# Optimization experiments

Hardware: AMD Instinct MI355X
Metric: run time of the kernel (lower is better)

The kernel has to match this reference:

```python
import jax, jax.numpy as jnp
import numpy as np

TOP_K = 2


def setup_inputs() -> dict:
    key = jax.random.key(0)
    ks = jax.random.split(key, 8)
    B, S, D, E = 4, 2048, 768, 8
    F = 4 * D
    scale = 0.02
    x = jax.random.normal(ks[0], (B, S, D), dtype=jnp.float32)
    router_w = jax.random.normal(ks[1], (D, E), dtype=jnp.float32) * scale
    router_b = jnp.zeros((E,), dtype=jnp.float32)
    w1 = jax.random.normal(ks[2], (E, D, F), dtype=jnp.float32) * scale
    b1 = jnp.zeros((E, F), dtype=jnp.float32)
    w2 = jax.random.normal(ks[3], (E, F, D), dtype=jnp.float32) * scale
    b2 = jnp.zeros((E, D), dtype=jnp.float32)
    return {"x": x, "router_w": router_w, "router_b": router_b,
            "w1": w1, "b1": b1, "w2": w2, "b2": b2}


def reference(x, router_w, router_b, w1, b1, w2, b2):
    E = w1.shape[0]
    # router: [B,S,E]
    logits = jnp.einsum('bsd,de->bse', x, router_w) + router_b
    probs = jax.nn.softmax(logits, axis=-1)
    top_p, top_i = jax.lax.top_k(probs, TOP_K)          # [B,S,K]
    top_p = top_p / jnp.sum(top_p, axis=-1, keepdims=True)
    # dense combine weights [B,S,E]: renormalized top-k prob if selected else 0
    combine = jnp.sum(jax.nn.one_hot(top_i, E, dtype=x.dtype) * top_p[..., None], axis=-2)
    # loop over small fixed expert count (structurally distinct weight slices)
    out = jnp.zeros_like(x)
    for e in range(E):
        h = jax.nn.gelu(jnp.einsum('bsd,df->bsf', x, w1[e]) + b1[e], approximate=False)
        y = jnp.einsum('bsf,fd->bsd', h, w2[e]) + b2[e]
        out = out + combine[..., e:e + 1] * y
    return out
```

## Files before the change

### kernel.cpp

```cpp
#include <hip/hip_runtime.h>
#include <hip/hip_bf16.h>
#include <math.h>

#define TOKENS 8192
#define Dm 768
#define Fm 3072
#define Em 8
#define BK 64
#define MT_MAX 71

typedef __attribute__((ext_vector_type(8))) short short8v;
typedef __attribute__((ext_vector_type(4))) short short4v;
typedef __attribute__((ext_vector_type(4))) float f32x4;

__device__ inline short f2b(float f) {
  __hip_bfloat16 h = __float2bfloat16(f);
  return *reinterpret_cast<short*>(&h);
}

__device__ inline void async16(short* lds, const short* g) {
  __builtin_amdgcn_global_load_lds((const __attribute__((address_space(1))) void*)g,
                                   (__attribute__((address_space(3))) void*)lds, 16, 0, 0);
}

__global__ __launch_bounds__(256) void cvt_tr_kernel(const float* __restrict__ in,
                                                     short* __restrict__ out, int R, int C) {
  __shared__ short tile[64][68];
  size_t eoff = (size_t)blockIdx.z * R * C;
  const float* inp = in + eoff;
  short* outp = out + eoff;
  int tc = blockIdx.x * 64, tr = blockIdx.y * 64;
  {
    int row = threadIdx.x >> 2;
    int cch = (threadIdx.x & 3) * 16;
    const float* src = inp + (size_t)(tr + row) * C + tc + cch;
    #pragma unroll
    for (int q = 0; q < 4; q++) {
      float4 v = *(const float4*)(src + q * 4);
      tile[row][cch + q * 4 + 0] = f2b(v.x);
      tile[row][cch + q * 4 + 1] = f2b(v.y);
      tile[row][cch + q * 4 + 2] = f2b(v.z);
      tile[row][cch + q * 4 + 3] = f2b(v.w);
    }
  }
  __syncthreads();
  {
    int c = threadIdx.x >> 2;
    int rch = (threadIdx.x & 3) * 16;
    short tmp[16];
    #pragma unroll
    for (int i = 0; i < 16; i++) tmp[i] = tile[rch + i][c];
    short* dst = outp + (size_t)(tc + c) * R + tr + rch;
    *(short8v*)(dst) = *(short8v*)(tmp);
    *(short8v*)(dst + 8) = *(short8v*)(tmp + 8);
  }
}

__global__ __launch_bounds__(256) void router_kernel(
    const float* __restrict__ x, const float* __restrict__ rw,
    const float* __restrict__ rb, const float* __restrict__ b2,
    short* __restrict__ xb, float* __restrict__ out,
    int2* __restrict__ meta_e, float2* __restrict__ meta_p) {
  int wave = threadIdx.x >> 6;
  int lane = threadIdx.x & 63;
  int t = blockIdx.x * 4 + wave;
  if (t >= TOKENS) return;
  const float* xr = x + (size_t)t * Dm;
  short* xbr = xb + (size_t)t * Dm;
  float acc[Em];
  #pragma unroll
  for (int e = 0; e < Em; e++) acc[e] = 0.f;
  #pragma unroll
  for (int i = 0; i < 3; i++) {
    int d = i * 256 + lane * 4;
    float4 v = *(const float4*)(xr + d);
    short4v s;
    s[0] = f2b(v.x); s[1] = f2b(v.y); s[2] = f2b(v.z); s[3] = f2b(v.w);
    *(short4v*)(xbr + d) = s;
    #pragma unroll
    for (int j = 0; j < 4; j++) {
      float xv = (j == 0) ? v.x : (j == 1) ? v.y : (j == 2) ? v.z : v.w;
      const float4* rwp = (const float4*)(rw + (size_t)(d + j) * Em);
      float4 a = rwp[0], b = rwp[1];
      acc[0] += xv * a.x; acc[1] += xv * a.y; acc[2] += xv * a.z; acc[3] += xv * a.w;
      acc[4] += xv * b.x; acc[5] += xv * b.y; acc[6] += xv * b.z; acc[7] += xv * b.w;
    }
  }
  #pragma unroll
  for (int e = 0; e < Em; e++) {
    float v = acc[e];
    #pragma unroll
    for (int s = 32; s > 0; s >>= 1) v += __shfl_xor(v, s);
    acc[e] = v + rb[e];
  }
  int i1 = 0; float m1 = acc[0];
  #pragma unroll
  for (int e = 1; e < Em; e++) if (acc[e] > m1) { m1 = acc[e]; i1 = e; }
  int i2 = -1; float m2 = -1e30f;
  #pragma unroll
  for (int e = 0; e < Em; e++) if (e != i1 && acc[e] > m2) { m2 = acc[e]; i2 = e; }
  float tt = expf(m2 - m1);
  float p0 = 1.f / (1.f + tt);
  float p1 = tt / (1.f + tt);
  const float4* ba = (const float4*)(b2 + (size_t)i1 * Dm);
  const float4* bb = (const float4*)(b2 + (size_t)i2 * Dm);
  float4* orow = (float4*)(out + (size_t)t * Dm);
  #pragma unroll
  for (int i = 0; i < 3; i++) {
    int idx = lane + 64 * i;
    float4 a = ba[idx], b = bb[idx];
    float4 o;
    o.x = p0 * a.x + p1 * b.x; o.y = p0 * a.y + p1 * b.y;
    o.z = p0 * a.z + p1 * b.z; o.w = p0 * a.w + p1 * b.w;
    orow[idx] = o;
  }
  if (lane == 0) {
    meta_e[t] = make_int2(i1, i2);
    meta_p[t] = make_float2(p0, p1);
  }
}

__global__ __launch_bounds__(256) void scatter_kernel(
    const int2* __restrict__ meta_e, const float2* __restrict__ meta_p,
    int* __restrict__ cnt, int* __restrict__ list, float* __restrict__ wlist) {
  __shared__ int lcnt[Em];
  __shared__ int gbase[Em];
  int t = blockIdx.x * 256 + threadIdx.x;
  if (threadIdx.x < Em) lcnt[threadIdx.x] = 0;
  __syncthreads();
  int2 e = meta_e[t];
  float2 p = meta_p[t];
  int r0 = atomicAdd(&lcnt[e.x], 1);
  int r1 = atomicAdd(&lcnt[e.y], 1);
  __syncthreads();
  if (threadIdx.x < Em) gbase[threadIdx.x] = atomicAdd(&cnt[threadIdx.x], lcnt[threadIdx.x]);
  __syncthreads();
  int s0 = gbase[e.x] + r0;
  int s1 = gbase[e.y] + r1;
  list[e.x * TOKENS + s0] = t;  wlist[e.x * TOKENS + s0] = p.x;
  list[e.y * TOKENS + s1] = t;  wlist[e.y * TOKENS + s1] = p.y;
}

__global__ void prefix_kernel(const int* __restrict__ cnt, int* __restrict__ hoffs,
                              int2* __restrict__ table, int* __restrict__ ntab) {
  if (threadIdx.x == 0) {
    int s = 0, k = 0;
    for (int e = 0; e < Em; e++) {
      hoffs[e] = s;
      int c = cnt[e];
      for (int mb = 0; mb < c; mb += 256) table[k++] = make_int2(e, mb);
      s += c;
    }
    ntab[0] = k;
  }
}

template <int MODE, int NB>
__global__ __launch_bounds__(512, 2) void moe_gemm_kernel(
    const short* __restrict__ Abase, const short* __restrict__ Wt,
    const float* __restrict__ bias, short* __restrict__ Hout,
    float* __restrict__ Out, const int* __restrict__ cnt,
    const int* __restrict__ hoffs, const int* __restrict__ list,
    const float* __restrict__ wlist, const int2* __restrict__ table,
    const int* __restrict__ ntab, int Ndim, int Kdim) {
  int nwg = gridDim.x;
  int orig = blockIdx.x;
  int q8 = nwg >> 3, r8 = nwg & 7, xcd = orig & 7;
  int wg = (xcd < r8 ? xcd * (q8 + 1) : r8 * (q8 + 1) + (xcd - r8) * q8) + (orig >> 3);
  int ti = wg / NB, nt = wg % NB;
  if (ti >= ntab[0]) return;
  int2 te = table[ti];
  int e = te.x, mbase = te.y;
  int count = cnt[e], ho = hoffs[e];
  int n0 = nt * 256;

  __shared__ short As[2][256 * 64];
  __shared__ short Bs[2][256 * 64];
  __shared__ int rid_s[256];
  __shared__ float pw_s[256];

  int tid = threadIdx.x;
  if (tid < 256) {
    int rc = mbase + tid; if (rc > count - 1) rc = count - 1;
    rid_s[tid] = list[e * TOKENS + rc];
    pw_s[tid] = wlist[e * TOKENS + rc];
  }
  __syncthreads();

  const short* We = Wt + (size_t)e * Ndim * Kdim;
  const short* aptr[4];
  const short* bptr[4];
  #pragma unroll
  for (int q = 0; q < 4; q++) {
    int r = q * 64 + (tid >> 3);
    int g = (tid & 7) ^ (r & 7);
    size_t grow;
    if (MODE == 0) {
      grow = (size_t)rid_s[r] * Kdim;
    } else {
      int rr = mbase + r; if (rr > count - 1) rr = count - 1;
      grow = (size_t)(ho + rr) * Kdim;
    }
    aptr[q] = Abase + grow + g * 8;
    bptr[q] = We + (size_t)(n0 + r) * Kdim + g * 8;
  }
  int w = tid >> 6;

  #define STAGE(s)                                             \
    {                                                          \
      _Pragma("unroll")                                        \
      for (int q = 0; q < 4; q++) {                            \
        async16(&As[s][q * 4096 + w * 512], aptr[q]); aptr[q] += BK; \
        async16(&Bs[s][q * 4096 + w * 512], bptr[q]); bptr[q] += BK; \
      }                                                        \
      __builtin_amdgcn_sched_barrier(0);                       \
    }

  int NT = Kdim / BK;
  f32x4 acc[8][4] = {};
  int lane = tid & 63;
  int wm = (tid >> 6) >> 2, wn = (tid >> 6) & 3;
  int lr = lane & 15, lh = lane >> 4;
  int rsw = lr & 7;

  STAGE(0);
  __syncthreads();
  for (int t = 0; t < NT; t++) {
    int cur = t & 1;
    if (t + 1 < NT) STAGE(cur ^ 1);
    const short* Ab = As[cur];
    const short* Bb = Bs[cur];
    #pragma unroll
    for (int kk = 0; kk < 2; kk++) {
      short8v a[8], b[4];
      #pragma unroll
      for (int m = 0; m < 8; m++)
        a[m] = *(const short8v*)&Ab[(wm * 128 + m * 16 + lr) * 64 + ((kk * 4 + lh) ^ rsw) * 8];
      #pragma unroll
      for (int n = 0; n < 4; n++)
        b[n] = *(const short8v*)&Bb[(wn * 64 + n * 16 + lr) * 64 + ((kk * 4 + lh) ^ rsw) * 8];
      #pragma unroll
      for (int m = 0; m < 8; m++)
        #pragma unroll
        for (int n = 0; n < 4; n++)
          acc[m][n] = __builtin_amdgcn_mfma_f32_16x16x32_bf16(a[m], b[n], acc[m][n], 0, 0, 0);
    }
    __syncthreads();
  }
  #undef STAGE

  if (MODE == 0) {
    const float* be = bias + (size_t)e * Ndim;
    #pragma unroll
    for (int m = 0; m < 8; m++) {
      #pragma unroll
      for (int j = 0; j < 4; j++) {
        int r = wm * 128 + m * 16 + lh * 4 + j;
        if (mbase + r < count) {
          size_t rowoff = (size_t)(ho + mbase + r) * Ndim;
          #pragma unroll
          for (int n = 0; n < 4; n++) {
            int colg = n0 + wn * 64 + n * 16 + lr;
            float val = acc[m][n][j] + be[colg];
            float z = val * 0.70710678118654752f;
            float az = fabsf(z);
            float tt = __fdividef(1.f, fmaf(0.3275911f, az, 1.f));
            float poly = fmaf(fmaf(fmaf(fmaf(1.061405429f, tt, -1.453152027f), tt,
                              1.421413741f), tt, -0.284496736f), tt, 0.254829592f) * tt;
            float er = 1.f - poly * __expf(-az * az);
            er = z < 0.f ? -er : er;
            val = 0.5f * val * (1.f + er);
            Hout[rowoff + colg] = f2b(val);
          }
        }
      }
    }
  } else {
    #pragma unroll
    for (int m = 0; m < 8; m++) {
      #pragma unroll
      for (int j = 0; j < 4; j++) {
        int r = wm * 128 + m * 16 + lh * 4 + j;
        if (mbase + r < count) {
          float* orow = Out + (size_t)rid_s[r] * Dm;
          float p = pw_s[r];
          #pragma unroll
          for (int n = 0; n < 4; n++) {
            int colg = n0 + wn * 64 + n * 16 + lr;
            atomicAdd(&orow[colg], p * acc[m][n][j]);
          }
        }
      }
    }
  }
}

extern "C" void kernel_launch(void* const* d_in, const int* in_sizes, int n_in,
                              void* d_out, int out_size, void* d_ws, size_t ws_size,
                              hipStream_t stream) {
  const float* x  = (const float*)d_in[0];
  const float* rw = (const float*)d_in[1];
  const float* rb = (const float*)d_in[2];
  const float* w1 = (const float*)d_in[3];
  const float* b1 = (const float*)d_in[4];
  const float* w2 = (const float*)d_in[5];
  const float* b2 = (const float*)d_in[6];
  float* out = (float*)d_out;
  char* ws = (char*)d_ws;

  const size_t off_cnt    = 0;
  const size_t off_hoffs  = 64;
  const size_t off_ntab   = 128;
  const size_t off_table  = 192;
  const size_t off_list   = 2048;
  const size_t off_wlist  = off_list + (size_t)Em * TOKENS * 4;
  const size_t off_meta_e = off_wlist + (size_t)Em * TOKENS * 4;
  const size_t off_meta_p = off_meta_e + (size_t)TOKENS * 8;
  const size_t off_xbf    = off_meta_p + (size_t)TOKENS * 8;
  const size_t off_w1t    = off_xbf + (size_t)TOKENS * Dm * 2;
  const size_t off_w2t    = off_w1t + (size_t)Em * Dm * Fm * 2;
  const size_t off_h      = off_w2t + (size_t)Em * Fm * Dm * 2;
  const size_t needed     = off_h + (size_t)2 * TOKENS * Fm * 2;
  if (ws_size < needed) return;

  int*    cnt    = (int*)(ws + off_cnt);
  int*    hoffs  = (int*)(ws + off_hoffs);
  int*    ntab   = (int*)(ws + off_ntab);
  int2*   table  = (int2*)(ws + off_table);
  int*    list   = (int*)(ws + off_list);
  float*  wlist  = (float*)(ws + off_wlist);
  int2*   meta_e = (int2*)(ws + off_meta_e);
  float2* meta_p = (float2*)(ws + off_meta_p);
  short*  xbf    = (short*)(ws + off_xbf);
  short*  w1t    = (short*)(ws + off_w1t);
  short*  w2t    = (short*)(ws + off_w2t);
  short*  h      = (short*)(ws + off_h);

  hipMemsetAsync(cnt, 0, 32, stream);
  cvt_tr_kernel<<<dim3(Fm / 64, Dm / 64, Em), 256, 0, stream>>>(w1, w1t, Dm, Fm);
  cvt_tr_kernel<<<dim3(Dm / 64, Fm / 64, Em), 256, 0, stream>>>(w2, w2t, Fm, Dm);
  router_kernel<<<TOKENS / 4, 256, 0, stream>>>(x, rw, rb, b2, xbf, out, meta_e, meta_p);
  scatter_kernel<<<TOKENS / 256, 256, 0, stream>>>(meta_e, meta_p, cnt, list, wlist);
  prefix_kernel<<<1, 64, 0, stream>>>(cnt, hoffs, table, ntab);
  moe_gemm_kernel<0, Fm / 256><<<MT_MAX * (Fm / 256), 512, 0, stream>>>(
      xbf, w1t, b1, h, nullptr, cnt, hoffs, list, wlist, table, ntab, Fm, Dm);
  moe_gemm_kernel<1, Dm / 256><<<MT_MAX * (Dm / 256), 512, 0, stream>>>(
      h, w2t, nullptr, nullptr, out, cnt, hoffs, list, wlist, table, ntab, Dm, Fm);
}
```

Measured before the change: 381.4 us.

## Shrink MoE GEMM tiles to 128x128 with pipelined split-k-step schedule

Shrinks the expert GEMM tiles from 256x256 with 512 threads to 128x128 with 256 threads, doubling the number of row tiles per expert so the grid has more, smaller workgroups. This is meant to cut padding waste on partially filled expert tiles and improve load balance. The main loop is restructured to issue both LDS stages up front, split each 64-wide k-step into two MFMA halves with priority hints, and place the barrier and next prefetch between the halves using explicit vmcnt waits. Smaller tiles lower per-block data reuse and increase weight re-reads from global memory.

```diff
diff --git a/kernel.cpp b/kernel.cpp
--- a/kernel.cpp
+++ b/kernel.cpp
@@ -7,7 +7,7 @@
 #define Fm 3072
 #define Em 8
 #define BK 64
-#define MT_MAX 71
+#define MT_MAX 136
 
 typedef __attribute__((ext_vector_type(8))) short short8v;
 typedef __attribute__((ext_vector_type(4))) short short4v;
@@ -148,7 +148,7 @@
     for (int e = 0; e < Em; e++) {
       hoffs[e] = s;
       int c = cnt[e];
-      for (int mb = 0; mb < c; mb += 256) table[k++] = make_int2(e, mb);
+      for (int mb = 0; mb < c; mb += 128) table[k++] = make_int2(e, mb);
       s += c;
     }
     ntab[0] = k;
@@ -156,7 +156,7 @@
 }
 
 template <int MODE, int NB>
-__global__ __launch_bounds__(512, 2) void moe_gemm_kernel(
+__global__ __launch_bounds__(256, 2) void moe_gemm_kernel(
     const short* __restrict__ Abase, const short* __restrict__ Wt,
     const float* __restrict__ bias, short* __restrict__ Hout,
     float* __restrict__ Out, const int* __restrict__ cnt,
@@ -172,15 +172,15 @@
   int2 te = table[ti];
   int e = te.x, mbase = te.y;
   int count = cnt[e], ho = hoffs[e];
-  int n0 = nt * 256;
-
-  __shared__ short As[2][256 * 64];
-  __shared__ short Bs[2][256 * 64];
-  __shared__ int rid_s[256];
-  __shared__ float pw_s[256];
+  int n0 = nt * 128;
+
+  __shared__ short As[2][128 * 64];
+  __shared__ short Bs[2][128 * 64];
+  __shared__ int rid_s[128];
+  __shared__ float pw_s[128];
 
   int tid = threadIdx.x;
-  if (tid < 256) {
+  if (tid < 128) {
     int rc = mbase + tid; if (rc > count - 1) rc = count - 1;
     rid_s[tid] = list[e * TOKENS + rc];
     pw_s[tid] = wlist[e * TOKENS + rc];
@@ -192,7 +192,7 @@
   const short* bptr[4];
   #pragma unroll
   for (int q = 0; q < 4; q++) {
-    int r = q * 64 + (tid >> 3);
+    int r = q * 32 + (tid >> 3);
     int g = (tid & 7) ^ (r & 7);
     size_t grow;
     if (MODE == 0) {
@@ -210,52 +210,74 @@
     {                                                          \
       _Pragma("unroll")                                        \
       for (int q = 0; q < 4; q++) {                            \
-        async16(&As[s][q * 4096 + w * 512], aptr[q]); aptr[q] += BK; \
-        async16(&Bs[s][q * 4096 + w * 512], bptr[q]); bptr[q] += BK; \
+        async16(&As[s][q * 2048 + w * 512], aptr[q]); aptr[q] += BK; \
+        async16(&Bs[s][q * 2048 + w * 512], bptr[q]); bptr[q] += BK; \
       }                                                        \
-      __builtin_amdgcn_sched_barrier(0);                       \
     }
 
   int NT = Kdim / BK;
-  f32x4 acc[8][4] = {};
+  f32x4 acc[4][4] = {};
   int lane = tid & 63;
-  int wm = (tid >> 6) >> 2, wn = (tid >> 6) & 3;
+  int wm = w >> 1, wn = w & 1;
   int lr = lane & 15, lh = lane >> 4;
   int rsw = lr & 7;
 
   STAGE(0);
-  __syncthreads();
+  STAGE(1);
+  asm volatile("s_waitcnt vmcnt(8)" ::: "memory");
+  __builtin_amdgcn_s_barrier();
+
   for (int t = 0; t < NT; t++) {
-    int cur = t & 1;
-    if (t + 1 < NT) STAGE(cur ^ 1);
-    const short* Ab = As[cur];
-    const short* Bb = Bs[cur];
-    #pragma unroll
-    for (int kk = 0; kk < 2; kk++) {
-      short8v a[8], b[4];
-      #pragma unroll
-      for (int m = 0; m < 8; m++)
-        a[m] = *(const short8v*)&Ab[(wm * 128 + m * 16 + lr) * 64 + ((kk * 4 + lh) ^ rsw) * 8];
+    int s = t & 1;
+    const short* Ab = As[s];
+    const short* Bb = Bs[s];
+    short8v a0[4], b0[4];
+    #pragma unroll
+    for (int m = 0; m < 4; m++)
+      a0[m] = *(const short8v*)&Ab[(wm * 64 + m * 16 + lr) * 64 + (lh ^ rsw) * 8];
+    #pragma unroll
+    for (int n = 0; n < 4; n++)
+      b0[n] = *(const short8v*)&Bb[(wn * 64 + n * 16 + lr) * 64 + (lh ^ rsw) * 8];
+    __builtin_amdgcn_s_setprio(1);
+    #pragma unroll
+    for (int m = 0; m < 4; m++)
       #pragma unroll
       for (int n = 0; n < 4; n++)
-        b[n] = *(const short8v*)&Bb[(wn * 64 + n * 16 + lr) * 64 + ((kk * 4 + lh) ^ rsw) * 8];
+        acc[m][n] = __builtin_amdgcn_mfma_f32_16x16x32_bf16(a0[m], b0[n], acc[m][n], 0, 0, 0);
+    __builtin_amdgcn_s_setprio(0);
+    short8v a1[4], b1v[4];
+    #pragma unroll
+    for (int m = 0; m < 4; m++)
+      a1[m] = *(const short8v*)&Ab[(wm * 64 + m * 16 + lr) * 64 + ((4 + lh) ^ rsw) * 8];
+    #pragma unroll
+    for (int n = 0; n < 4; n++)
+      b1v[n] = *(const short8v*)&Bb[(wn * 64 + n * 16 + lr) * 64 + ((4 + lh) ^ rsw) * 8];
+    asm volatile("s_waitcnt lgkmcnt(0)" ::: "memory");
+    __builtin_amdgcn_sched_barrier(0);
+    __builtin_amdgcn_s_barrier();
+    if (t + 2 < NT) STAGE(s);
+    __builtin_amdgcn_s_setprio(1);
+    #pragma unroll
+    for (int m = 0; m < 4; m++)
       #pragma unroll
-      for (int m = 0; m < 8; m++)
-        #pragma unroll
-        for (int n = 0; n < 4; n++)
-          acc[m][n] = __builtin_amdgcn_mfma_f32_16x16x32_bf16(a[m], b[n], acc[m][n], 0, 0, 0);
-    }
-    __syncthreads();
+      for (int n = 0; n < 4; n++)
+        acc[m][n] = __builtin_amdgcn_mfma_f32_16x16x32_bf16(a1[m], b1v[n], acc[m][n], 0, 0, 0);
+    __builtin_amdgcn_s_setprio(0);
+    if (t + 2 < NT)
+      asm volatile("s_waitcnt vmcnt(8)" ::: "memory");
+    else
+      asm volatile("s_waitcnt vmcnt(0)" ::: "memory");
+    __builtin_amdgcn_s_barrier();
   }
   #undef STAGE
 
   if (MODE == 0) {
     const float* be = bias + (size_t)e * Ndim;
     #pragma unroll
-    for (int m = 0; m < 8; m++) {
+    for (int m = 0; m < 4; m++) {
       #pragma unroll
       for (int j = 0; j < 4; j++) {
-        int r = wm * 128 + m * 16 + lh * 4 + j;
+        int r = wm * 64 + m * 16 + lh * 4 + j;
         if (mbase + r < count) {
           size_t rowoff = (size_t)(ho + mbase + r) * Ndim;
           #pragma unroll
@@ -277,10 +299,10 @@
     }
   } else {
     #pragma unroll
-    for (int m = 0; m < 8; m++) {
+    for (int m = 0; m < 4; m++) {
       #pragma unroll
       for (int j = 0; j < 4; j++) {
-        int r = wm * 128 + m * 16 + lh * 4 + j;
+        int r = wm * 64 + m * 16 + lh * 4 + j;
         if (mbase + r < count) {
           float* orow = Out + (size_t)rid_s[r] * Dm;
           float p = pw_s[r];
@@ -342,8 +364,8 @@
   router_kernel<<<TOKENS / 4, 256, 0, stream>>>(x, rw, rb, b2, xbf, out, meta_e, meta_p);
   scatter_kernel<<<TOKENS / 256, 256, 0, stream>>>(meta_e, meta_p, cnt, list, wlist);
   prefix_kernel<<<1, 64, 0, stream>>>(cnt, hoffs, table, ntab);
-  moe_gemm_kernel<0, Fm / 256><<<MT_MAX * (Fm / 256), 512, 0, stream>>>(
+  moe_gemm_kernel<0, Fm / 128><<<MT_MAX * (Fm / 128), 256, 0, stream>>>(
       xbf, w1t, b1, h, nullptr, cnt, hoffs, list, wlist, table, ntab, Fm, Dm);
-  moe_gemm_kernel<1, Dm / 256><<<MT_MAX * (Dm / 256), 512, 0, stream>>>(
+  moe_gemm_kernel<1, Dm / 128><<<MT_MAX * (Dm / 128), 256, 0, stream>>>(
       h, w2t, nullptr, nullptr, out, cnt, hoffs, list, wlist, table, ntab, Dm, Fm);
 }
```

Measured after the change: 362.6 us. -4.9%, faster.
